# Kernel tuning notes

Hardware: AMD Instinct MI355X
Metric: run time of the kernel (lower is better)

The kernel has to match this reference:

```python
import jax, jax.numpy as jnp
import numpy as np

B, C, H, W = 8, 512, 64, 64
D = C // 8  # 64

def setup_inputs() -> dict:
    key = jax.random.key(0)
    ks = jax.random.split(key, 10)
    s = 0.02
    return {
        "x":  jax.random.normal(ks[0], (B, C, H, W), dtype=jnp.float32),
        "Wq": jax.random.normal(ks[1], (D, C), dtype=jnp.float32) * s,
        "bq": jnp.zeros((D,), dtype=jnp.float32),
        "Wk": jax.random.normal(ks[2], (D, C), dtype=jnp.float32) * s,
        "bk": jnp.zeros((D,), dtype=jnp.float32),
        "Wv": jax.random.normal(ks[3], (D, C), dtype=jnp.float32) * s,
        "bv": jnp.zeros((D,), dtype=jnp.float32),
        "Wo": jax.random.normal(ks[4], (C, D), dtype=jnp.float32) * s,
        "bo": jnp.zeros((C,), dtype=jnp.float32),
        "gamma": jnp.full((1,), 0.5, dtype=jnp.float32),
    }

def reference(x, Wq, bq, Wk, bk, Wv, bv, Wo, bo, gamma):
    b, c, h, w = x.shape
    n = h * w
    xf = x.reshape(b, c, n)                                   # (B, C, N)
    # 1x1 convs == channel matmuls (spectral_norm only reparametrizes the weight)
    q = jnp.einsum('dc,bcn->bnd', Wq, xf) + bq                # (B, N, D)
    k = jnp.einsum('dc,bcn->bdn', Wk, xf) + bk[:, None]       # (B, D, N)
    v = jnp.einsum('dc,bcn->bdn', Wv, xf) + bv[:, None]       # (B, D, N)
    # unscaled scores, softmax over key index (last dim)
    attn = jax.nn.softmax(jnp.einsum('bnd,bdm->bnm', q, k), axis=-1)  # (B, N, N)
    out = jnp.einsum('bdm,bnm->bdn', v, attn)                 # (B, D, N)
    out = jnp.einsum('cd,bdn->bcn', Wo, out) + bo[:, None]    # (B, C, N)
    return (out * gamma + xf).reshape(b, c, h, w)
```

## Files before the change

### kernel.cpp

```cpp
#include <hip/hip_runtime.h>
#include <hip/hip_bf16.h>

#define DEVFN __device__ __forceinline__

typedef __bf16 bf16x8 __attribute__((ext_vector_type(8)));
typedef float f32x4 __attribute__((ext_vector_type(4)));
typedef float float4_t __attribute__((ext_vector_type(4)));
typedef unsigned short ushort8_t __attribute__((ext_vector_type(8)));
typedef unsigned short ushort4_t __attribute__((ext_vector_type(4)));
typedef unsigned int uint4_t __attribute__((ext_vector_type(4)));

constexpr int Bd = 8, Cd = 512, Nd = 4096, Dd = 64;

DEVFN unsigned short f2bf(float f) {
    union { float f; unsigned int u; } v; v.f = f;
    unsigned int r = (v.u + 0x7FFFu + ((v.u >> 16) & 1u)) >> 16;
    return (unsigned short)r;
}

DEVFN unsigned int pack2(float a, float b) {
    __hip_bfloat162 h = __float22bfloat162_rn(make_float2(a, b));
    union { __hip_bfloat162 h; unsigned int u; } c; c.h = h;
    return c.u;
}

DEVFN bf16x8 ld_bf8(const unsigned short* p) {
    ushort8_t u = *(const ushort8_t*)p;
    return __builtin_bit_cast(bf16x8, u);
}

DEVFN f32x4 mfma16(bf16x8 a, bf16x8 b, f32x4 c) {
    return __builtin_amdgcn_mfma_f32_16x16x32_bf16(a, b, c, 0, 0, 0);
}

__global__ __launch_bounds__(256) void k_cvtw(
    const float* __restrict__ Wq, const float* __restrict__ Wk,
    const float* __restrict__ Wv, const float* __restrict__ Wo,
    unsigned short* __restrict__ w4)
{
    int i = blockIdx.x * 256 + threadIdx.x;
    w4[i]          = f2bf(Wq[i]);
    w4[32768 + i]  = f2bf(Wk[i]);
    w4[65536 + i]  = f2bf(Wv[i]);
    w4[98304 + i]  = f2bf(Wo[i]);
}

__global__ __launch_bounds__(512, 2) void k_qkv(
    const float* __restrict__ x,
    const unsigned short* __restrict__ wq,
    const unsigned short* __restrict__ wk,
    const unsigned short* __restrict__ wv,
    const float* __restrict__ bq, const float* __restrict__ bk, const float* __restrict__ bv,
    unsigned short* __restrict__ q_nd, unsigned short* __restrict__ k_nd,
    unsigned short* __restrict__ v_dn)
{
    const int b   = blockIdx.y;
    const int n0  = blockIdx.x * 128;
    const int tid = threadIdx.x, wid = tid >> 6, l = tid & 63;
    const int lo  = l & 15, hi = l >> 4;
    const float* xb = x + (size_t)b * Cd * Nd;

    __shared__ __align__(16) unsigned short sm[2][64][136];

    f32x4 acc[12] = {};

    const int lrow = l >> 5;
    const int lcol = (l & 31) * 4;
    float4_t xrA[4], xrB[4];

    auto gloadA = [&](int t) {
        const int c0 = t * 64;
        #pragma unroll
        for (int i = 0; i < 4; ++i)
            xrA[i] = *(const float4_t*)(xb + (size_t)(c0 + wid*8 + lrow + i*2) * Nd + n0 + lcol);
    };
    auto gloadB = [&](int t) {
        const int c0 = t * 64;
        #pragma unroll
        for (int i = 0; i < 4; ++i)
            xrB[i] = *(const float4_t*)(xb + (size_t)(c0 + wid*8 + lrow + i*2) * Nd + n0 + lcol);
    };
    const int wswz = (wid & 3) * 8;
    auto dswriteA = [&](int buf) {
        #pragma unroll
        for (int i = 0; i < 4; ++i) {
            const int rl = wid*8 + lrow + i*2;
            ushort4_t u;
            #pragma unroll
            for (int j = 0; j < 4; ++j) u[j] = f2bf(xrA[i][j]);
            *(ushort4_t*)&sm[buf][rl][lcol ^ wswz] = u;
        }
    };
    auto dswriteB = [&](int buf) {
        #pragma unroll
        for (int i = 0; i < 4; ++i) {
            const int rl = wid*8 + lrow + i*2;
            ushort4_t u;
            #pragma unroll
            for (int j = 0; j < 4; ++j) u[j] = f2bf(xrB[i][j]);
            *(ushort4_t*)&sm[buf][rl][lcol ^ wswz] = u;
        }
    };
    auto compute = [&](int buf, int t) {
        #pragma unroll
        for (int kk = 0; kk < 2; ++kk) {
            const int rc = (wid*16 + lo) ^ (hi*8);
            ushort8_t ua;
            #pragma unroll
            for (int j = 0; j < 8; ++j)
                ua[j] = sm[buf][kk*32 + hi*8 + j][rc];
            bf16x8 af = __builtin_bit_cast(bf16x8, ua);
            #pragma unroll
            for (int jj = 0; jj < 12; ++jj) {
                const unsigned short* wm = (jj < 4) ? wq : (jj < 8) ? wk : wv;
                const int d0 = (jj & 3) * 16;
                bf16x8 bf = ld_bf8(wm + (d0 + lo) * Cd + t*64 + kk*32 + hi*8);
                acc[jj] = mfma16(af, bf, acc[jj]);
            }
        }
    };

    gloadA(0);
    dswriteA(0);
    gloadB(1);
    __syncthreads();
    for (int t = 0; t < 8; t += 2) {
        if (t + 2 < 8) gloadA(t + 2);
        __builtin_amdgcn_sched_barrier(0);
        compute(0, t);
        dswriteB(1);
        __syncthreads();
        if (t + 3 < 8) gloadB(t + 3);
        __builtin_amdgcn_sched_barrier(0);
        compute(1, t + 1);
        if (t + 2 < 8) dswriteA(0);
        __syncthreads();
    }

    unsigned short* epi = &sm[0][0][0];
    unsigned short* tl  = epi + wid * 16 * 72;
    #pragma unroll
    for (int m = 0; m < 2; ++m) {
        const float* bias = m ? bk : bq;
        #pragma unroll
        for (int jj = 0; jj < 4; ++jj) {
            const float bia = bias[jj*16 + lo];
            #pragma unroll
            for (int r = 0; r < 4; ++r)
                tl[(hi*4 + r) * 72 + jj*16 + lo] = f2bf(acc[m*4 + jj][r] + bia);
        }
        asm volatile("" ::: "memory");
        const int row = l >> 2, dg = l & 3;
        ushort8_t a0 = *(const ushort8_t*)&tl[row*72 + dg*16];
        ushort8_t a1 = *(const ushort8_t*)&tl[row*72 + dg*16 + 8];
        unsigned short* dst = (m ? k_nd : q_nd)
            + ((size_t)b * Nd + n0 + wid*16 + row) * 64 + dg*16;
        *(ushort8_t*)dst = a0; *(ushort8_t*)(dst + 8) = a1;
        asm volatile("" ::: "memory");
    }
    __syncthreads();

    unsigned short* vt2 = &sm[0][0][0];
    #pragma unroll
    for (int jj = 0; jj < 4; ++jj) {
        const float bia = bv[jj*16 + lo];
        #pragma unroll
        for (int r = 0; r < 4; ++r)
            vt2[(jj*16 + lo) * 136 + wid*16 + hi*4 + r] = f2bf(acc[8 + jj][r] + bia);
    }
    __syncthreads();
    {
        const int d = tid >> 3, nc = (tid & 7) * 16;
        ushort8_t a0 = *(const ushort8_t*)&vt2[d*136 + nc];
        ushort8_t a1 = *(const ushort8_t*)&vt2[d*136 + nc + 8];
        unsigned short* dst = v_dn + ((size_t)b * Dd + d) * Nd + n0 + nc;
        *(ushort8_t*)dst = a0; *(ushort8_t*)(dst + 8) = a1;
    }
}

__global__ __launch_bounds__(512, 4) void k_attn(
    const unsigned short* __restrict__ q_nd,
    const unsigned short* __restrict__ k_nd,
    const unsigned short* __restrict__ v_dn,
    unsigned short* __restrict__ o_nd)
{
    const int bid = blockIdx.x;
    const int b   = bid & 7;
    const int n0  = (bid >> 3) * 64;
    const int tid = threadIdx.x, wid = tid >> 6, l = tid & 63;
    const int lo  = l & 15, hi = l >> 4;
    const int lsw = lo & 7;
    const int qh  = wid >> 2;
    const int kh  = (wid >> 1) & 1;
    const int tp  = wid & 1;
    const int wk0 = kh * 32;

    __shared__ __align__(16) unsigned short kv_lds[2][2][2][64 * 64];
    __shared__ float red_l[3][2][2][16];

    const unsigned short* qb = q_nd + (size_t)b * Nd * Dd;
    const unsigned short* kb = k_nd + (size_t)b * Nd * Dd;
    const unsigned short* vb = v_dn + (size_t)b * Dd * Nd;

    bf16x8 aq[2][2];
    #pragma unroll
    for (int qs = 0; qs < 2; ++qs)
        #pragma unroll
        for (int kc = 0; kc < 2; ++kc)
            aq[qs][kc] = ld_bf8(qb + (size_t)(n0 + qh*32 + qs*16 + lo) * 64 + kc*32 + hi*8);

    f32x4 acc[2][4] = {};
    float l_p[2] = {0.f, 0.f};

    const int sr = tid >> 3, ss = tid & 7;
    const int kwsl = (ss ^ (sr & 7)) * 8;
    const int vkh = ss >> 2, vsl = ss & 3, vms = vsl >> 1;
    const int vg0 = vkh * 4 + ((2 * vsl) & 3);
    const int vg1 = vkh * 4 + ((2 * vsl + 1) & 3);
    const int vsw = sr & 7;
    ushort8_t kr0, kr1, vr0, vr1;

    auto gload = [&](int it) {
        const size_t m1 = (size_t)it * 128;
        kr0 = *(const ushort8_t*)(kb + (m1 + sr) * 64 + ss * 8);
        kr1 = *(const ushort8_t*)(kb + (m1 + 64 + sr) * 64 + ss * 8);
        vr0 = *(const ushort8_t*)(vb + (size_t)sr * Nd + m1 + ss * 8);
        vr1 = *(const ushort8_t*)(vb + (size_t)sr * Nd + m1 + 64 + ss * 8);
    };
    auto dswrite = [&](int buf) {
        unsigned short* kt0 = &kv_lds[0][buf][0][0];
        unsigned short* kt1 = &kv_lds[0][buf][1][0];
        unsigned short* vt0 = &kv_lds[1][buf][0][0];
        unsigned short* vt1 = &kv_lds[1][buf][1][0];
        *(ushort8_t*)(kt0 + sr * 64 + kwsl) = kr0;
        *(ushort8_t*)(kt1 + sr * 64 + kwsl) = kr1;
        ushort4_t a0 = __builtin_shufflevector(vr0, vr0, 0, 1, 2, 3);
        ushort4_t a1 = __builtin_shufflevector(vr0, vr0, 4, 5, 6, 7);
        ushort4_t b0 = __builtin_shufflevector(vr1, vr1, 0, 1, 2, 3);
        ushort4_t b1 = __builtin_shufflevector(vr1, vr1, 4, 5, 6, 7);
        *(ushort4_t*)(vt0 + sr * 64 + (vg0 ^ vsw) * 8 + vms * 4) = a0;
        *(ushort4_t*)(vt0 + sr * 64 + (vg1 ^ vsw) * 8 + vms * 4) = a1;
        *(ushort4_t*)(vt1 + sr * 64 + (vg0 ^ vsw) * 8 + vms * 4) = b0;
        *(ushort4_t*)(vt1 + sr * 64 + (vg1 ^ vsw) * 8 + vms * 4) = b1;
    };

    auto compute = [&](int buf) {
        const unsigned short* kt = &kv_lds[0][buf][tp][0];
        const unsigned short* vt = &kv_lds[1][buf][tp][0];
        f32x4 s[2][2] = {};
        #pragma unroll
        for (int ms = 0; ms < 2; ++ms) {
            #pragma unroll
            for (int kc = 0; kc < 2; ++kc) {
                bf16x8 kf = ld_bf8(kt + (wk0 + ms*16 + lo) * 64 + (((kc*4 + hi) ^ lsw) * 8));
                #pragma unroll
                for (int qs = 0; qs < 2; ++qs)
                    s[qs][ms] = mfma16(kf, aq[qs][kc], s[qs][ms]);
            }
        }
        bf16x8 vf[4];
        #pragma unroll
        for (int ds = 0; ds < 4; ++ds)
            vf[ds] = ld_bf8(vt + (ds*16 + lo) * 64 + (((kh*4 + hi) ^ lsw) * 8));
        #pragma unroll
        for (int qs = 0; qs < 2; ++qs) {
            float p[2][4];
            #pragma unroll
            for (int ms = 0; ms < 2; ++ms)
                #pragma unroll
                for (int r = 0; r < 4; ++r)
                    p[ms][r] = __expf(s[qs][ms][r]);
            l_p[qs] += ((p[0][0] + p[0][1]) + (p[0][2] + p[0][3]))
                     + ((p[1][0] + p[1][1]) + (p[1][2] + p[1][3]));
            uint4_t w;
            w[0] = pack2(p[0][0], p[0][1]);
            w[1] = pack2(p[0][2], p[0][3]);
            w[2] = pack2(p[1][0], p[1][1]);
            w[3] = pack2(p[1][2], p[1][3]);
            bf16x8 apf = __builtin_bit_cast(bf16x8, w);
            #pragma unroll
            for (int ds = 0; ds < 4; ++ds)
                acc[qs][ds] = mfma16(apf, vf[ds], acc[qs][ds]);
        }
    };

    constexpr int NIT = Nd / 128;
    gload(0);
    dswrite(0);
    __syncthreads();
    for (int it = 0; it < NIT; ++it) {
        const int cur = it & 1;
        if (it + 1 < NIT) gload(it + 1);
        __builtin_amdgcn_sched_barrier(0);
        compute(cur);
        if (it + 1 < NIT) dswrite(cur ^ 1);
        __syncthreads();
    }

    float lh[2];
    #pragma unroll
    for (int qs = 0; qs < 2; ++qs) {
        float ps = l_p[qs];
        ps += __shfl_xor(ps, 16, 64);
        ps += __shfl_xor(ps, 32, 64);
        lh[qs] = ps;
    }
    float* red = (float*)&kv_lds[0][0][0][0];
    const int g = (kh * 2 + tp) - 1;
    if (g >= 0) {
        #pragma unroll
        for (int qs = 0; qs < 2; ++qs) {
            #pragma unroll
            for (int ds = 0; ds < 4; ++ds) {
                const int idx = ((g * 2 + qh) * 2 + qs) * 4 + ds;
                *(f32x4*)&red[idx * 256 + l * 4] = acc[qs][ds];
            }
            red_l[g][qh][qs][lo] = lh[qs];
        }
    }
    __syncthreads();
    if (g < 0) {
        #pragma unroll
        for (int qs = 0; qs < 2; ++qs) {
            #pragma unroll
            for (int gg = 0; gg < 3; ++gg) {
                #pragma unroll
                for (int ds = 0; ds < 4; ++ds) {
                    const int idx = ((gg * 2 + qh) * 2 + qs) * 4 + ds;
                    acc[qs][ds] += *(const f32x4*)&red[idx * 256 + l * 4];
                }
                lh[qs] += red_l[gg][qh][qs][lo];
            }
            #pragma unroll
            for (int r = 0; r < 4; ++r) {
                float lq = __shfl(lh[qs], hi * 4 + r, 16);
                float rl = 1.0f / lq;
                #pragma unroll
                for (int ds = 0; ds < 4; ++ds) {
                    float o = acc[qs][ds][r] * rl;
                    o_nd[((size_t)b * Nd + n0 + qh*32 + qs*16 + hi*4 + r) * 64 + ds*16 + lo] = f2bf(o);
                }
            }
        }
    }
}

__global__ __launch_bounds__(256) void k_oproj(
    const unsigned short* __restrict__ o_nd,
    const unsigned short* __restrict__ wo,
    const float* __restrict__ bo,
    const float* __restrict__ gamma,
    const float* __restrict__ x,
    float* __restrict__ out)
{
    const int b   = blockIdx.y;
    const int n0  = blockIdx.x * 64;
    const int tid = threadIdx.x, wid = tid >> 6, l = tid & 63;
    const int lo  = l & 15, hi = l >> 4;
    const int n0w = n0 + wid * 16;
    const float g = gamma[0];

    bf16x8 ao[2];
    #pragma unroll
    for (int kc = 0; kc < 2; ++kc)
        ao[kc] = ld_bf8(o_nd + ((size_t)b * Nd + n0w + lo) * 64 + kc*32 + hi*8);

    for (int ct = 0; ct < 32; ++ct) {
        f32x4 acc = {};
        #pragma unroll
        for (int kc = 0; kc < 2; ++kc) {
            bf16x8 bw = ld_bf8(wo + (ct*16 + lo) * 64 + kc*32 + hi*8);
            acc = mfma16(ao[kc], bw, acc);
        }
        const int c = ct*16 + lo;
        const float bc = bo[c];
        const size_t base = ((size_t)b * Cd + c) * Nd + n0w + hi*4;
        float4_t xv = *(const float4_t*)(x + base);
        float4_t ov;
        #pragma unroll
        for (int r = 0; r < 4; ++r) ov[r] = g * (acc[r] + bc) + xv[r];
        *(float4_t*)(out + base) = ov;
    }
}

extern "C" void kernel_launch(void* const* d_in, const int* in_sizes, int n_in,
                              void* d_out, int out_size, void* d_ws, size_t ws_size,
                              hipStream_t stream) {
    (void)in_sizes; (void)n_in; (void)out_size; (void)ws_size;
    const float* x  = (const float*)d_in[0];
    const float* Wq = (const float*)d_in[1];
    const float* bq = (const float*)d_in[2];
    const float* Wk = (const float*)d_in[3];
    const float* bk = (const float*)d_in[4];
    const float* Wv = (const float*)d_in[5];
    const float* bv = (const float*)d_in[6];
    const float* Wo = (const float*)d_in[7];
    const float* bo = (const float*)d_in[8];
    const float* gm = (const float*)d_in[9];
    float* out = (float*)d_out;

    unsigned short* w4   = (unsigned short*)d_ws;
    unsigned short* q_nd = w4 + 131072;
    unsigned short* k_nd = q_nd + (size_t)Bd * Nd * Dd;
    unsigned short* v_dn = k_nd + (size_t)Bd * Nd * Dd;
    unsigned short* o_nd = v_dn + (size_t)Bd * Nd * Dd;

    k_cvtw<<<128, 256, 0, stream>>>(Wq, Wk, Wv, Wo, w4);
    dim3 gq(Nd / 128, Bd);
    k_qkv<<<gq, 512, 0, stream>>>(x, w4, w4 + 32768, w4 + 65536, bq, bk, bv, q_nd, k_nd, v_dn);
    k_attn<<<512, 512, 0, stream>>>(q_nd, k_nd, v_dn, o_nd);
    dim3 g1(Nd / 64, Bd);
    k_oproj<<<g1, 256, 0, stream>>>(o_nd, w4 + 98304, bo, gm, x, out);
}
```

Measured before the change: 147.5 us.

## Restructure QKV projection to load full channel slab into LDS up front

The QKV projection kernel now uses 64-column tiles with 256 threads and 512 blocks instead of 128-column tiles with 512 threads. Each block loads its whole 512-channel slab of x into 64 KB of LDS (as bf16, XOR-swizzled) in two large batches, then runs all MFMA steps with no per-step syncs. This replaces the double-buffered pipeline and aims for more memory parallelism and more blocks. The cost is higher LDS use per block, which may cap occupancy, and no overlap between loading and compute within a block.

```diff
diff --git a/kernel.cpp b/kernel.cpp
--- a/kernel.cpp
+++ b/kernel.cpp
@@ -45,7 +45,7 @@
     w4[98304 + i]  = f2bf(Wo[i]);
 }
 
-__global__ __launch_bounds__(512, 2) void k_qkv(
+__global__ __launch_bounds__(256, 2) void k_qkv(
     const float* __restrict__ x,
     const unsigned short* __restrict__ wq,
     const unsigned short* __restrict__ wk,
@@ -55,125 +55,95 @@
     unsigned short* __restrict__ v_dn)
 {
     const int b   = blockIdx.y;
-    const int n0  = blockIdx.x * 128;
+    const int n0  = blockIdx.x * 64;
     const int tid = threadIdx.x, wid = tid >> 6, l = tid & 63;
     const int lo  = l & 15, hi = l >> 4;
-    const float* xb = x + (size_t)b * Cd * Nd;
-
-    __shared__ __align__(16) unsigned short sm[2][64][136];
+    const float* xb = x + (size_t)b * Cd * Nd + n0;
+
+    __shared__ __align__(16) unsigned short sm[512 * 64];
+
+    const int lr = tid >> 4;
+    const int nc = (tid & 15) * 4;
+    #pragma unroll
+    for (int half = 0; half < 2; ++half) {
+        float4_t xr[16];
+        #pragma unroll
+        for (int r = 0; r < 16; ++r) {
+            const int c = half * 256 + r * 16 + lr;
+            xr[r] = *(const float4_t*)(xb + (size_t)c * Nd + nc);
+        }
+        __builtin_amdgcn_sched_barrier(0);
+        #pragma unroll
+        for (int r = 0; r < 16; ++r) {
+            const int c = half * 256 + r * 16 + lr;
+            const int s = ((c >> 3) & 3) << 4;
+            ushort4_t u;
+            #pragma unroll
+            for (int j = 0; j < 4; ++j) u[j] = f2bf(xr[r][j]);
+            *(ushort4_t*)&sm[c * 64 + (nc ^ s)] = u;
+        }
+    }
+    __syncthreads();
 
     f32x4 acc[12] = {};
-
-    const int lrow = l >> 5;
-    const int lcol = (l & 31) * 4;
-    float4_t xrA[4], xrB[4];
-
-    auto gloadA = [&](int t) {
-        const int c0 = t * 64;
-        #pragma unroll
-        for (int i = 0; i < 4; ++i)
-            xrA[i] = *(const float4_t*)(xb + (size_t)(c0 + wid*8 + lrow + i*2) * Nd + n0 + lcol);
-    };
-    auto gloadB = [&](int t) {
-        const int c0 = t * 64;
-        #pragma unroll
-        for (int i = 0; i < 4; ++i)
-            xrB[i] = *(const float4_t*)(xb + (size_t)(c0 + wid*8 + lrow + i*2) * Nd + n0 + lcol);
-    };
-    const int wswz = (wid & 3) * 8;
-    auto dswriteA = [&](int buf) {
-        #pragma unroll
-        for (int i = 0; i < 4; ++i) {
-            const int rl = wid*8 + lrow + i*2;
-            ushort4_t u;
-            #pragma unroll
-            for (int j = 0; j < 4; ++j) u[j] = f2bf(xrA[i][j]);
-            *(ushort4_t*)&sm[buf][rl][lcol ^ wswz] = u;
-        }
-    };
-    auto dswriteB = [&](int buf) {
-        #pragma unroll
-        for (int i = 0; i < 4; ++i) {
-            const int rl = wid*8 + lrow + i*2;
-            ushort4_t u;
-            #pragma unroll
-            for (int j = 0; j < 4; ++j) u[j] = f2bf(xrB[i][j]);
-            *(ushort4_t*)&sm[buf][rl][lcol ^ wswz] = u;
-        }
-    };
-    auto compute = [&](int buf, int t) {
+    for (int t = 0; t < 8; ++t) {
         #pragma unroll
         for (int kk = 0; kk < 2; ++kk) {
-            const int rc = (wid*16 + lo) ^ (hi*8);
+            const int cbase = t * 64 + kk * 32 + hi * 8;
+            const int s   = ((cbase >> 3) & 3) << 4;
+            const int col = (wid * 16 + lo) ^ s;
             ushort8_t ua;
             #pragma unroll
             for (int j = 0; j < 8; ++j)
-                ua[j] = sm[buf][kk*32 + hi*8 + j][rc];
+                ua[j] = sm[(cbase + j) * 64 + col];
             bf16x8 af = __builtin_bit_cast(bf16x8, ua);
             #pragma unroll
             for (int jj = 0; jj < 12; ++jj) {
                 const unsigned short* wm = (jj < 4) ? wq : (jj < 8) ? wk : wv;
                 const int d0 = (jj & 3) * 16;
-                bf16x8 bf = ld_bf8(wm + (d0 + lo) * Cd + t*64 + kk*32 + hi*8);
+                bf16x8 bf = ld_bf8(wm + (d0 + lo) * Cd + t * 64 + kk * 32 + hi * 8);
                 acc[jj] = mfma16(af, bf, acc[jj]);
             }
         }
-    };
-
-    gloadA(0);
-    dswriteA(0);
-    gloadB(1);
-    __syncthreads();
-    for (int t = 0; t < 8; t += 2) {
-        if (t + 2 < 8) gloadA(t + 2);
-        __builtin_amdgcn_sched_barrier(0);
-        compute(0, t);
-        dswriteB(1);
-        __syncthreads();
-        if (t + 3 < 8) gloadB(t + 3);
-        __builtin_amdgcn_sched_barrier(0);
-        compute(1, t + 1);
-        if (t + 2 < 8) dswriteA(0);
-        __syncthreads();
-    }
-
-    unsigned short* epi = &sm[0][0][0];
-    unsigned short* tl  = epi + wid * 16 * 72;
+    }
+    __syncthreads();
+
+    unsigned short* tl = sm + wid * (16 * 72);
     #pragma unroll
     for (int m = 0; m < 2; ++m) {
         const float* bias = m ? bk : bq;
         #pragma unroll
         for (int jj = 0; jj < 4; ++jj) {
-            const float bia = bias[jj*16 + lo];
+            const float bia = bias[jj * 16 + lo];
             #pragma unroll
             for (int r = 0; r < 4; ++r)
-                tl[(hi*4 + r) * 72 + jj*16 + lo] = f2bf(acc[m*4 + jj][r] + bia);
+                tl[(hi * 4 + r) * 72 + jj * 16 + lo] = f2bf(acc[m * 4 + jj][r] + bia);
         }
         asm volatile("" ::: "memory");
         const int row = l >> 2, dg = l & 3;
-        ushort8_t a0 = *(const ushort8_t*)&tl[row*72 + dg*16];
-        ushort8_t a1 = *(const ushort8_t*)&tl[row*72 + dg*16 + 8];
+        ushort8_t a0 = *(const ushort8_t*)&tl[row * 72 + dg * 16];
+        ushort8_t a1 = *(const ushort8_t*)&tl[row * 72 + dg * 16 + 8];
         unsigned short* dst = (m ? k_nd : q_nd)
-            + ((size_t)b * Nd + n0 + wid*16 + row) * 64 + dg*16;
+            + ((size_t)b * Nd + n0 + wid * 16 + row) * 64 + dg * 16;
         *(ushort8_t*)dst = a0; *(ushort8_t*)(dst + 8) = a1;
         asm volatile("" ::: "memory");
     }
     __syncthreads();
 
-    unsigned short* vt2 = &sm[0][0][0];
+    unsigned short* vt = sm;
     #pragma unroll
     for (int jj = 0; jj < 4; ++jj) {
-        const float bia = bv[jj*16 + lo];
+        const float bia = bv[jj * 16 + lo];
         #pragma unroll
         for (int r = 0; r < 4; ++r)
-            vt2[(jj*16 + lo) * 136 + wid*16 + hi*4 + r] = f2bf(acc[8 + jj][r] + bia);
+            vt[(jj * 16 + lo) * 72 + wid * 16 + hi * 4 + r] = f2bf(acc[8 + jj][r] + bia);
     }
     __syncthreads();
     {
-        const int d = tid >> 3, nc = (tid & 7) * 16;
-        ushort8_t a0 = *(const ushort8_t*)&vt2[d*136 + nc];
-        ushort8_t a1 = *(const ushort8_t*)&vt2[d*136 + nc + 8];
-        unsigned short* dst = v_dn + ((size_t)b * Dd + d) * Nd + n0 + nc;
+        const int d = tid >> 2, ng = tid & 3;
+        ushort8_t a0 = *(const ushort8_t*)&vt[d * 72 + ng * 16];
+        ushort8_t a1 = *(const ushort8_t*)&vt[d * 72 + ng * 16 + 8];
+        unsigned short* dst = v_dn + ((size_t)b * Dd + d) * Nd + n0 + ng * 16;
         *(ushort8_t*)dst = a0; *(ushort8_t*)(dst + 8) = a1;
     }
 }
@@ -406,8 +376,8 @@
     unsigned short* o_nd = v_dn + (size_t)Bd * Nd * Dd;
 
     k_cvtw<<<128, 256, 0, stream>>>(Wq, Wk, Wv, Wo, w4);
-    dim3 gq(Nd / 128, Bd);
-    k_qkv<<<gq, 512, 0, stream>>>(x, w4, w4 + 32768, w4 + 65536, bq, bk, bv, q_nd, k_nd, v_dn);
+    dim3 gq(Nd / 64, Bd);
+    k_qkv<<<gq, 256, 0, stream>>>(x, w4, w4 + 32768, w4 + 65536, bq, bk, bv, q_nd, k_nd, v_dn);
     k_attn<<<512, 512, 0, stream>>>(q_nd, k_nd, v_dn, o_nd);
     dim3 g1(Nd / 64, Bd);
     k_oproj<<<g1, 256, 0, stream>>>(o_nd, w4 + 98304, bo, gm, x, out);
```

After: 141.9 us, median of 2. 3.8% less time.
